# Performance work log

Measured on AMD Instinct MI355X. Metric: run time of the kernel, lower is better.

Reference implementation:

```python
import jax, jax.numpy as jnp
import numpy as np

D = 1024      # hidden_dim
E = 8         # num_experts
F = 512       # expert_dim


def setup_inputs() -> dict:
    key = jax.random.key(0)
    ks = jax.random.split(key, 7)
    B, N = 4, 4096
    s1 = 1.0 / np.sqrt(D)
    s2 = 1.0 / np.sqrt(F)
    return {
        "x": jax.random.normal(ks[0], (B, N, D), dtype=jnp.float32),
        "W1": jax.random.uniform(ks[1], (E, D, F), jnp.float32, -s1, s1),  # per-expert first linear
        "b1": jax.random.uniform(ks[2], (E, F), jnp.float32, -s1, s1),
        "W2": jax.random.uniform(ks[3], (E, F, D), jnp.float32, -s2, s2),  # per-expert second linear
        "b2": jax.random.uniform(ks[4], (E, D), jnp.float32, -s2, s2),
        "Wr": jax.random.uniform(ks[5], (D, E), jnp.float32, -s1, s1),    # router
        "br": jax.random.uniform(ks[6], (E,), jnp.float32, -s1, s1),
    }


def reference(x, W1, b1, W2, b2, Wr, br):
    # Router: softmax over experts per token. [B,N,E]
    router_weights = jax.nn.softmax(x @ Wr + br, axis=-1)
    # All experts on all tokens (dense soft-MoE), batched as grouped GEMMs.
    h = jax.nn.gelu(jnp.einsum('bnd,edf->bnef', x, W1) + b1, approximate=False)  # [B,N,E,F]
    y = jnp.einsum('bnef,efd->bned', h, W2) + b2[None, None]                      # [B,N,E,D]
    # Softmax-weighted combine over experts.
    return jnp.einsum('bned,bne->bnd', y, router_weights)
```

## Files before the change

### kernel.cpp

```cpp
#include <hip/hip_runtime.h>
#include <hip/hip_bf16.h>
#include <math.h>

#define MTOK 16384
#define DDIM 1024
#define EEXP 8
#define FDIM 512
#define EFK  4096

typedef __attribute__((ext_vector_type(8))) short short8;
typedef __attribute__((ext_vector_type(4))) float floatx4;

__device__ __forceinline__ void gld_lds16(const void* g, void* l) {
  __builtin_amdgcn_global_load_lds((const __attribute__((address_space(1))) void*)g,
                                   (__attribute__((address_space(3))) void*)l, 16, 0, 0);
}

__device__ __forceinline__ float gelu_fast(float v) {
  const float z  = v * 0.70710678118654752f;
  const float az = fabsf(z);
  const float t  = __builtin_amdgcn_rcpf(1.f + 0.3275911f * az);
  const float poly = t * (0.254829592f +
                     t * (-0.284496736f +
                     t * (1.421413741f +
                     t * (-1.453152027f +
                     t * 1.061405429f))));
  const float ex = __expf(-az * az);
  float erfv = 1.f - poly * ex;
  erfv = copysignf(erfv, z);
  return 0.5f * v * (1.f + erfv);
}

__global__ __launch_bounds__(256) void transpose_cast_kernel(
    const float* __restrict__ in, __hip_bfloat16* __restrict__ out, int R, int C) {
  __shared__ float tile[32][33];
  const float* inb = in + (size_t)blockIdx.z * R * C;
  __hip_bfloat16* outb = out + (size_t)blockIdx.z * R * C;
  const int c0 = blockIdx.x * 32, r0 = blockIdx.y * 32;
  const int tx = threadIdx.x & 31, ty = threadIdx.x >> 5;
#pragma unroll
  for (int i = 0; i < 4; ++i)
    tile[ty + i * 8][tx] = inb[(size_t)(r0 + ty + i * 8) * C + (c0 + tx)];
  __syncthreads();
#pragma unroll
  for (int i = 0; i < 4; ++i)
    outb[(size_t)(c0 + ty + i * 8) * R + (r0 + tx)] = __float2bfloat16(tile[tx][ty + i * 8]);
}

__global__ __launch_bounds__(256) void router_cast_kernel(
    const float* __restrict__ x, const float* __restrict__ Wr, const float* __restrict__ br,
    __hip_bfloat16* __restrict__ xbf, float* __restrict__ r) {
  const int wave = (blockIdx.x * 256 + threadIdx.x) >> 6;
  const int lane = threadIdx.x & 63;
  const float* xr = x + (size_t)wave * DDIM;
  float acc[EEXP];
#pragma unroll
  for (int e = 0; e < EEXP; ++e) acc[e] = 0.f;
#pragma unroll
  for (int i = 0; i < DDIM / 64; ++i) {
    const int d = i * 64 + lane;
    const float xv = xr[d];
    xbf[(size_t)wave * DDIM + d] = __float2bfloat16(xv);
    const float4* w4 = (const float4*)(Wr + (size_t)d * EEXP);
    const float4 w0 = w4[0], w1 = w4[1];
    acc[0] += xv * w0.x; acc[1] += xv * w0.y; acc[2] += xv * w0.z; acc[3] += xv * w0.w;
    acc[4] += xv * w1.x; acc[5] += xv * w1.y; acc[6] += xv * w1.z; acc[7] += xv * w1.w;
  }
#pragma unroll
  for (int off = 32; off; off >>= 1) {
#pragma unroll
    for (int e = 0; e < EEXP; ++e) acc[e] += __shfl_xor(acc[e], off, 64);
  }
  float mx = -1e30f;
#pragma unroll
  for (int e = 0; e < EEXP; ++e) { acc[e] += br[e]; mx = fmaxf(mx, acc[e]); }
  float s = 0.f;
#pragma unroll
  for (int e = 0; e < EEXP; ++e) { acc[e] = expf(acc[e] - mx); s += acc[e]; }
  const float inv = 1.f / s;
  if (lane < EEXP) r[(size_t)wave * EEXP + lane] = acc[lane] * inv;
}

__global__ __launch_bounds__(256, 4) void gemm_h_kernel(
    const __hip_bfloat16* __restrict__ A, const __hip_bfloat16* __restrict__ W1t,
    const float* __restrict__ b1, const float* __restrict__ r,
    __hip_bfloat16* __restrict__ Hs) {
  const int e  = blockIdx.z;
  const int M0 = blockIdx.x * 128;
  const int N0 = blockIdx.y * 128;
  const __hip_bfloat16* Be = W1t + (size_t)e * FDIM * DDIM;

  __shared__ __hip_bfloat16 sA[2][128 * 32];
  __shared__ __hip_bfloat16 sB[2][128 * 32];

  const int tid  = threadIdx.x;
  const int lane = tid & 63;
  const int wid  = tid >> 6;
  const int wf = (wid >> 1) * 64;
  const int wt = (wid & 1) * 64;
  const int srow = tid >> 2;
  const int scol = (tid & 3) * 8;
  const int laneq = lane >> 4;
  const int lanem = lane & 15;

  floatx4 acc[4][4];
#pragma unroll
  for (int i = 0; i < 4; ++i)
#pragma unroll
    for (int j = 0; j < 4; ++j) acc[i][j] = (floatx4){0.f, 0.f, 0.f, 0.f};

  const __hip_bfloat16* ga0 = A  + (size_t)(M0 + srow)      * DDIM + scol;
  const __hip_bfloat16* ga1 = A  + (size_t)(M0 + 64 + srow) * DDIM + scol;
  const __hip_bfloat16* gb0 = Be + (size_t)(N0 + srow)      * DDIM + scol;
  const __hip_bfloat16* gb1 = Be + (size_t)(N0 + 64 + srow) * DDIM + scol;

#define STAGE1(p, k0)                                         \
  do {                                                        \
    gld_lds16(ga0 + (k0), &sA[p][(size_t)tid * 8]);           \
    gld_lds16(ga1 + (k0), &sA[p][2048 + (size_t)tid * 8]);    \
    gld_lds16(gb0 + (k0), &sB[p][(size_t)tid * 8]);           \
    gld_lds16(gb1 + (k0), &sB[p][2048 + (size_t)tid * 8]);    \
  } while (0)

  STAGE1(0, 0);
  const int KT = DDIM / 32;
  for (int kt = 0; kt < KT; ++kt) {
    const int p = kt & 1;
    __syncthreads();
    if (kt + 1 < KT) STAGE1(p ^ 1, (kt + 1) * 32);
    short8 wfr[4], xfr[4];
#pragma unroll
    for (int i = 0; i < 4; ++i) wfr[i] = *(const short8*)(&sB[p][(wf + i * 16 + lanem) * 32 + laneq * 8]);
#pragma unroll
    for (int j = 0; j < 4; ++j) xfr[j] = *(const short8*)(&sA[p][(wt + j * 16 + lanem) * 32 + laneq * 8]);
#pragma unroll
    for (int i = 0; i < 4; ++i)
#pragma unroll
      for (int j = 0; j < 4; ++j)
        acc[i][j] = __builtin_amdgcn_mfma_f32_16x16x32_bf16(wfr[i], xfr[j], acc[i][j], 0, 0, 0);
  }
#undef STAGE1

#pragma unroll
  for (int j = 0; j < 4; ++j) {
    const int tok = M0 + wt + j * 16 + lanem;
    const float rv = r[(size_t)tok * EEXP + e];
#pragma unroll
    for (int i = 0; i < 4; ++i) {
      const int f0 = wf + i * 16 + laneq * 4;
      const float4 b4 = *(const float4*)(b1 + e * FDIM + N0 + f0);
      union { ushort4 u; __hip_bfloat16 h[4]; } pk;
      pk.h[0] = __float2bfloat16(gelu_fast(acc[i][j][0] + b4.x) * rv);
      pk.h[1] = __float2bfloat16(gelu_fast(acc[i][j][1] + b4.y) * rv);
      pk.h[2] = __float2bfloat16(gelu_fast(acc[i][j][2] + b4.z) * rv);
      pk.h[3] = __float2bfloat16(gelu_fast(acc[i][j][3] + b4.w) * rv);
      *(ushort4*)(Hs + (size_t)tok * EFK + e * FDIM + N0 + f0) = pk.u;
    }
  }
}

__global__ __launch_bounds__(256, 4) void gemm_out_kernel(
    const __hip_bfloat16* __restrict__ Hs, const __hip_bfloat16* __restrict__ W2t,
    const float* __restrict__ b2, const float* __restrict__ r,
    float* __restrict__ out) {
  const int M0 = blockIdx.x * 128;
  const int N0 = blockIdx.y * 128;

  __shared__ __hip_bfloat16 sA[2][128 * 32];
  __shared__ __hip_bfloat16 sB[2][128 * 32];

  const int tid  = threadIdx.x;
  const int lane = tid & 63;
  const int wid  = tid >> 6;
  const int wf = (wid >> 1) * 64;
  const int wt = (wid & 1) * 64;
  const int srow = tid >> 2;
  const int scol = (tid & 3) * 8;
  const int laneq = lane >> 4;
  const int lanem = lane & 15;

  floatx4 acc[4][4];
#pragma unroll
  for (int i = 0; i < 4; ++i)
#pragma unroll
    for (int j = 0; j < 4; ++j) acc[i][j] = (floatx4){0.f, 0.f, 0.f, 0.f};

  const __hip_bfloat16* ga0 = Hs  + (size_t)(M0 + srow)      * EFK + scol;
  const __hip_bfloat16* ga1 = Hs  + (size_t)(M0 + 64 + srow) * EFK + scol;
  const __hip_bfloat16* gb0 = W2t + (size_t)(N0 + srow)      * EFK + scol;
  const __hip_bfloat16* gb1 = W2t + (size_t)(N0 + 64 + srow) * EFK + scol;

#define STAGE2(p, k0)                                         \
  do {                                                        \
    gld_lds16(ga0 + (k0), &sA[p][(size_t)tid * 8]);           \
    gld_lds16(ga1 + (k0), &sA[p][2048 + (size_t)tid * 8]);    \
    gld_lds16(gb0 + (k0), &sB[p][(size_t)tid * 8]);           \
    gld_lds16(gb1 + (k0), &sB[p][2048 + (size_t)tid * 8]);    \
  } while (0)

  STAGE2(0, 0);
  const int KT = EFK / 32;
  for (int kt = 0; kt < KT; ++kt) {
    const int p = kt & 1;
    __syncthreads();
    if (kt + 1 < KT) STAGE2(p ^ 1, (kt + 1) * 32);
    short8 wfr[4], hfr[4];
#pragma unroll
    for (int i = 0; i < 4; ++i) wfr[i] = *(const short8*)(&sB[p][(wf + i * 16 + lanem) * 32 + laneq * 8]);
#pragma unroll
    for (int j = 0; j < 4; ++j) hfr[j] = *(const short8*)(&sA[p][(wt + j * 16 + lanem) * 32 + laneq * 8]);
#pragma unroll
    for (int i = 0; i < 4; ++i)
#pragma unroll
      for (int j = 0; j < 4; ++j)
        acc[i][j] = __builtin_amdgcn_mfma_f32_16x16x32_bf16(wfr[i], hfr[j], acc[i][j], 0, 0, 0);
  }
#undef STAGE2

#pragma unroll
  for (int i = 0; i < 4; ++i) {
    const int d0 = N0 + wf + i * 16 + laneq * 4;
    float4 b2v[EEXP];
#pragma unroll
    for (int e = 0; e < EEXP; ++e) b2v[e] = *(const float4*)(b2 + e * DDIM + d0);
#pragma unroll
    for (int j = 0; j < 4; ++j) {
      const int tok = M0 + wt + j * 16 + lanem;
      const float4* r4 = (const float4*)(r + (size_t)tok * EEXP);
      const float4 r0 = r4[0], r1 = r4[1];
      const float rv[EEXP] = {r0.x, r0.y, r0.z, r0.w, r1.x, r1.y, r1.z, r1.w};
      float bx = 0.f, by = 0.f, bz = 0.f, bw = 0.f;
#pragma unroll
      for (int e = 0; e < EEXP; ++e) {
        bx += rv[e] * b2v[e].x; by += rv[e] * b2v[e].y;
        bz += rv[e] * b2v[e].z; bw += rv[e] * b2v[e].w;
      }
      float4 o;
      o.x = acc[i][j][0] + bx; o.y = acc[i][j][1] + by;
      o.z = acc[i][j][2] + bz; o.w = acc[i][j][3] + bw;
      *(float4*)(out + (size_t)tok * DDIM + d0) = o;
    }
  }
}

extern "C" void kernel_launch(void* const* d_in, const int* in_sizes, int n_in,
                              void* d_out, int out_size, void* d_ws, size_t ws_size,
                              hipStream_t stream) {
  const float* x  = (const float*)d_in[0];
  const float* W1 = (const float*)d_in[1];
  const float* b1 = (const float*)d_in[2];
  const float* W2 = (const float*)d_in[3];
  const float* b2 = (const float*)d_in[4];
  const float* Wr = (const float*)d_in[5];
  const float* br = (const float*)d_in[6];
  float* out = (float*)d_out;

  char* ws = (char*)d_ws;
  __hip_bfloat16* xbf = (__hip_bfloat16*)(ws);
  __hip_bfloat16* W1t = (__hip_bfloat16*)(ws + (32u << 20));
  __hip_bfloat16* W2t = (__hip_bfloat16*)(ws + (40u << 20));
  float*          r   = (float*)(ws + (48u << 20));
  __hip_bfloat16* Hs  = (__hip_bfloat16*)(ws + (48u << 20) + (1u << 19));

  transpose_cast_kernel<<<dim3(FDIM / 32, DDIM / 32, EEXP), 256, 0, stream>>>(W1, W1t, DDIM, FDIM);
  transpose_cast_kernel<<<dim3(DDIM / 32, EFK / 32, 1), 256, 0, stream>>>(W2, W2t, EFK, DDIM);
  router_cast_kernel<<<MTOK / 4, 256, 0, stream>>>(x, Wr, br, xbf, r);
  gemm_h_kernel<<<dim3(MTOK / 128, FDIM / 128, EEXP), 256, 0, stream>>>(xbf, W1t, b1, r, Hs);
  gemm_out_kernel<<<dim3(MTOK / 128, DDIM / 128), 256, 0, stream>>>(Hs, W2t, b2, r, out);
}
```

Measured before the change: 561.0 us.

## Enlarge GEMM block tiles to 128x256 with 512 threads and reorder out grid

Both expert GEMMs now use 512-thread blocks of eight waves that compute 128-token by 256-feature tiles from a single shared LDS buffer. This halves how often each activation tile is re-read per output tile, cutting global and L2 traffic. The output GEMM grid is flattened so that the four column tiles of one token block run next to each other, which should improve L2 reuse of the Hs rows. In exchange, LDS per block grows to 48 KB and the aggressive launch bounds (512, 6) can squeeze the register budget, which risks spills or lower occupancy.

```diff
diff --git a/kernel.cpp b/kernel.cpp
--- a/kernel.cpp
+++ b/kernel.cpp
@@ -81,27 +81,33 @@
   if (lane < EEXP) r[(size_t)wave * EEXP + lane] = acc[lane] * inv;
 }
 
-__global__ __launch_bounds__(256, 4) void gemm_h_kernel(
+
+#define TILE_A_ELEMS (128 * 32)
+#define TILE_ELEMS   ((128 + 256) * 32)
+
+__global__ __launch_bounds__(512, 6) void gemm_h_kernel(
     const __hip_bfloat16* __restrict__ A, const __hip_bfloat16* __restrict__ W1t,
     const float* __restrict__ b1, const float* __restrict__ r,
     __hip_bfloat16* __restrict__ Hs) {
+  const int M0 = blockIdx.x * 128;
+  const int F0 = blockIdx.y * 256;
   const int e  = blockIdx.z;
-  const int M0 = blockIdx.x * 128;
-  const int N0 = blockIdx.y * 128;
-  const __hip_bfloat16* Be = W1t + (size_t)e * FDIM * DDIM;
-
-  __shared__ __hip_bfloat16 sA[2][128 * 32];
-  __shared__ __hip_bfloat16 sB[2][128 * 32];
+
+  __shared__ __hip_bfloat16 lds[2][TILE_ELEMS];
 
   const int tid  = threadIdx.x;
   const int lane = tid & 63;
   const int wid  = tid >> 6;
-  const int wf = (wid >> 1) * 64;
-  const int wt = (wid & 1) * 64;
-  const int srow = tid >> 2;
-  const int scol = (tid & 3) * 8;
+  const int fg = (wid >> 1) * 64;
+  const int tg = (wid & 1) * 64;
   const int laneq = lane >> 4;
   const int lanem = lane & 15;
+  const int srow = tid >> 2;
+  const int cc8  = (tid & 3) * 8;
+
+  const __hip_bfloat16* gA = A + (size_t)(M0 + srow) * DDIM + cc8;
+  const __hip_bfloat16* gB = W1t + (size_t)e * FDIM * DDIM + (size_t)(F0 + srow) * DDIM + cc8;
+  const __hip_bfloat16* gB2 = gB + (size_t)128 * DDIM;
 
   floatx4 acc[4][4];
 #pragma unroll
@@ -109,75 +115,74 @@
 #pragma unroll
     for (int j = 0; j < 4; ++j) acc[i][j] = (floatx4){0.f, 0.f, 0.f, 0.f};
 
-  const __hip_bfloat16* ga0 = A  + (size_t)(M0 + srow)      * DDIM + scol;
-  const __hip_bfloat16* ga1 = A  + (size_t)(M0 + 64 + srow) * DDIM + scol;
-  const __hip_bfloat16* gb0 = Be + (size_t)(N0 + srow)      * DDIM + scol;
-  const __hip_bfloat16* gb1 = Be + (size_t)(N0 + 64 + srow) * DDIM + scol;
-
-#define STAGE1(p, k0)                                         \
-  do {                                                        \
-    gld_lds16(ga0 + (k0), &sA[p][(size_t)tid * 8]);           \
-    gld_lds16(ga1 + (k0), &sA[p][2048 + (size_t)tid * 8]);    \
-    gld_lds16(gb0 + (k0), &sB[p][(size_t)tid * 8]);           \
-    gld_lds16(gb1 + (k0), &sB[p][2048 + (size_t)tid * 8]);    \
+#define STAGEH(p, k0)                                               \
+  do {                                                              \
+    gld_lds16(gA  + (k0), &lds[p][(size_t)tid * 8]);                \
+    gld_lds16(gB  + (k0), &lds[p][(size_t)(512 + tid) * 8]);        \
+    gld_lds16(gB2 + (k0), &lds[p][(size_t)(1024 + tid) * 8]);       \
   } while (0)
 
-  STAGE1(0, 0);
+  STAGEH(0, 0);
   const int KT = DDIM / 32;
   for (int kt = 0; kt < KT; ++kt) {
     const int p = kt & 1;
     __syncthreads();
-    if (kt + 1 < KT) STAGE1(p ^ 1, (kt + 1) * 32);
+    if (kt + 1 < KT) STAGEH(p ^ 1, (kt + 1) * 32);
     short8 wfr[4], xfr[4];
 #pragma unroll
-    for (int i = 0; i < 4; ++i) wfr[i] = *(const short8*)(&sB[p][(wf + i * 16 + lanem) * 32 + laneq * 8]);
-#pragma unroll
-    for (int j = 0; j < 4; ++j) xfr[j] = *(const short8*)(&sA[p][(wt + j * 16 + lanem) * 32 + laneq * 8]);
+    for (int i = 0; i < 4; ++i)
+      wfr[i] = *(const short8*)(&lds[p][TILE_A_ELEMS + (fg + i * 16 + lanem) * 32 + laneq * 8]);
+#pragma unroll
+    for (int j = 0; j < 4; ++j)
+      xfr[j] = *(const short8*)(&lds[p][(tg + j * 16 + lanem) * 32 + laneq * 8]);
 #pragma unroll
     for (int i = 0; i < 4; ++i)
 #pragma unroll
       for (int j = 0; j < 4; ++j)
         acc[i][j] = __builtin_amdgcn_mfma_f32_16x16x32_bf16(wfr[i], xfr[j], acc[i][j], 0, 0, 0);
   }
-#undef STAGE1
+#undef STAGEH
 
 #pragma unroll
   for (int j = 0; j < 4; ++j) {
-    const int tok = M0 + wt + j * 16 + lanem;
+    const int tok = M0 + tg + j * 16 + lanem;
     const float rv = r[(size_t)tok * EEXP + e];
 #pragma unroll
     for (int i = 0; i < 4; ++i) {
-      const int f0 = wf + i * 16 + laneq * 4;
-      const float4 b4 = *(const float4*)(b1 + e * FDIM + N0 + f0);
+      const int f = F0 + fg + i * 16 + laneq * 4;
+      const float4 b4 = *(const float4*)(b1 + e * FDIM + f);
       union { ushort4 u; __hip_bfloat16 h[4]; } pk;
       pk.h[0] = __float2bfloat16(gelu_fast(acc[i][j][0] + b4.x) * rv);
       pk.h[1] = __float2bfloat16(gelu_fast(acc[i][j][1] + b4.y) * rv);
       pk.h[2] = __float2bfloat16(gelu_fast(acc[i][j][2] + b4.z) * rv);
       pk.h[3] = __float2bfloat16(gelu_fast(acc[i][j][3] + b4.w) * rv);
-      *(ushort4*)(Hs + (size_t)tok * EFK + e * FDIM + N0 + f0) = pk.u;
+      *(ushort4*)(Hs + (size_t)tok * EFK + e * FDIM + f) = pk.u;
     }
   }
 }
 
-__global__ __launch_bounds__(256, 4) void gemm_out_kernel(
+__global__ __launch_bounds__(512, 4) void gemm_out_kernel(
     const __hip_bfloat16* __restrict__ Hs, const __hip_bfloat16* __restrict__ W2t,
     const float* __restrict__ b2, const float* __restrict__ r,
     float* __restrict__ out) {
-  const int M0 = blockIdx.x * 128;
-  const int N0 = blockIdx.y * 128;
-
-  __shared__ __hip_bfloat16 sA[2][128 * 32];
-  __shared__ __hip_bfloat16 sB[2][128 * 32];
+  const int M0 = (blockIdx.x >> 2) * 128;
+  const int N0 = (blockIdx.x & 3) * 256;
+
+  __shared__ __hip_bfloat16 lds[2][TILE_ELEMS];
 
   const int tid  = threadIdx.x;
   const int lane = tid & 63;
   const int wid  = tid >> 6;
-  const int wf = (wid >> 1) * 64;
-  const int wt = (wid & 1) * 64;
-  const int srow = tid >> 2;
-  const int scol = (tid & 3) * 8;
+  const int dg = (wid >> 1) * 64;
+  const int tg = (wid & 1) * 64;
   const int laneq = lane >> 4;
   const int lanem = lane & 15;
+  const int srow = tid >> 2;
+  const int cc8  = (tid & 3) * 8;
+
+  const __hip_bfloat16* gA = Hs + (size_t)(M0 + srow) * EFK + cc8;
+  const __hip_bfloat16* gB = W2t + (size_t)(N0 + srow) * EFK + cc8;
+  const __hip_bfloat16* gB2 = gB + (size_t)128 * EFK;
 
   floatx4 acc[4][4];
 #pragma unroll
@@ -185,47 +190,43 @@
 #pragma unroll
     for (int j = 0; j < 4; ++j) acc[i][j] = (floatx4){0.f, 0.f, 0.f, 0.f};
 
-  const __hip_bfloat16* ga0 = Hs  + (size_t)(M0 + srow)      * EFK + scol;
-  const __hip_bfloat16* ga1 = Hs  + (size_t)(M0 + 64 + srow) * EFK + scol;
-  const __hip_bfloat16* gb0 = W2t + (size_t)(N0 + srow)      * EFK + scol;
-  const __hip_bfloat16* gb1 = W2t + (size_t)(N0 + 64 + srow) * EFK + scol;
-
-#define STAGE2(p, k0)                                         \
-  do {                                                        \
-    gld_lds16(ga0 + (k0), &sA[p][(size_t)tid * 8]);           \
-    gld_lds16(ga1 + (k0), &sA[p][2048 + (size_t)tid * 8]);    \
-    gld_lds16(gb0 + (k0), &sB[p][(size_t)tid * 8]);           \
-    gld_lds16(gb1 + (k0), &sB[p][2048 + (size_t)tid * 8]);    \
+#define STAGEO(p, k0)                                               \
+  do {                                                              \
+    gld_lds16(gA  + (k0), &lds[p][(size_t)tid * 8]);                \
+    gld_lds16(gB  + (k0), &lds[p][(size_t)(512 + tid) * 8]);        \
+    gld_lds16(gB2 + (k0), &lds[p][(size_t)(1024 + tid) * 8]);       \
   } while (0)
 
-  STAGE2(0, 0);
+  STAGEO(0, 0);
   const int KT = EFK / 32;
   for (int kt = 0; kt < KT; ++kt) {
     const int p = kt & 1;
     __syncthreads();
-    if (kt + 1 < KT) STAGE2(p ^ 1, (kt + 1) * 32);
+    if (kt + 1 < KT) STAGEO(p ^ 1, (kt + 1) * 32);
     short8 wfr[4], hfr[4];
 #pragma unroll
-    for (int i = 0; i < 4; ++i) wfr[i] = *(const short8*)(&sB[p][(wf + i * 16 + lanem) * 32 + laneq * 8]);
-#pragma unroll
-    for (int j = 0; j < 4; ++j) hfr[j] = *(const short8*)(&sA[p][(wt + j * 16 + lanem) * 32 + laneq * 8]);
+    for (int i = 0; i < 4; ++i)
+      wfr[i] = *(const short8*)(&lds[p][TILE_A_ELEMS + (dg + i * 16 + lanem) * 32 + laneq * 8]);
+#pragma unroll
+    for (int j = 0; j < 4; ++j)
+      hfr[j] = *(const short8*)(&lds[p][(tg + j * 16 + lanem) * 32 + laneq * 8]);
 #pragma unroll
     for (int i = 0; i < 4; ++i)
 #pragma unroll
       for (int j = 0; j < 4; ++j)
         acc[i][j] = __builtin_amdgcn_mfma_f32_16x16x32_bf16(wfr[i], hfr[j], acc[i][j], 0, 0, 0);
   }
-#undef STAGE2
+#undef STAGEO
 
 #pragma unroll
   for (int i = 0; i < 4; ++i) {
-    const int d0 = N0 + wf + i * 16 + laneq * 4;
+    const int d0 = N0 + dg + i * 16 + laneq * 4;
     float4 b2v[EEXP];
 #pragma unroll
     for (int e = 0; e < EEXP; ++e) b2v[e] = *(const float4*)(b2 + e * DDIM + d0);
 #pragma unroll
     for (int j = 0; j < 4; ++j) {
-      const int tok = M0 + wt + j * 16 + lanem;
+      const int tok = M0 + tg + j * 16 + lanem;
       const float4* r4 = (const float4*)(r + (size_t)tok * EEXP);
       const float4 r0 = r4[0], r1 = r4[1];
       const float rv[EEXP] = {r0.x, r0.y, r0.z, r0.w, r1.x, r1.y, r1.z, r1.w};
@@ -265,6 +266,6 @@
   transpose_cast_kernel<<<dim3(FDIM / 32, DDIM / 32, EEXP), 256, 0, stream>>>(W1, W1t, DDIM, FDIM);
   transpose_cast_kernel<<<dim3(DDIM / 32, EFK / 32, 1), 256, 0, stream>>>(W2, W2t, EFK, DDIM);
   router_cast_kernel<<<MTOK / 4, 256, 0, stream>>>(x, Wr, br, xbf, r);
-  gemm_h_kernel<<<dim3(MTOK / 128, FDIM / 128, EEXP), 256, 0, stream>>>(xbf, W1t, b1, r, Hs);
-  gemm_out_kernel<<<dim3(MTOK / 128, DDIM / 128), 256, 0, stream>>>(Hs, W2t, b2, r, out);
-}
+  gemm_h_kernel<<<dim3(MTOK / 128, FDIM / 256, EEXP), 512, 0, stream>>>(xbf, W1t, b1, r, Hs);
+  gemm_out_kernel<<<dim3((MTOK / 128) * (DDIM / 256)), 512, 0, stream>>>(Hs, W2t, b2, r, out);
+}
```

New measurement: 924.9 us. 64.9% more time.
